# Kernel tuning notes

Measured on AMD Instinct MI355X. Metric: run time of the kernel, lower is better.

## Reference

```python
import jax, jax.numpy as jnp
import numpy as np

H, CM, CS = 8, 16, 32  # num_heads, hidden_mv_channels, hidden_s_channels
_INNER_IDX = np.array([0, 2, 3, 4, 8, 9, 10, 14])  # PGA multivector components without e0


def _make_basis():
    # 9 Pin(3,0,1)-equivariant linear maps on 16-dim multivectors:
    # 5 grade projections + 4 left-multiplications by e0 (grade k -> grade k+1 e0-blades).
    # Component order: [1, e0, e1, e2, e3, e01, e02, e03, e12, e13, e23, e012, e013, e023, e123, e0123]
    b = np.zeros((9, 16, 16), dtype=np.float32)
    grades = [[0], [1, 2, 3, 4], [5, 6, 7, 8, 9, 10], [11, 12, 13, 14], [15]]
    for k, idxs in enumerate(grades):
        for i in idxs:
            b[k, i, i] = 1.0
    e0maps = {5: [(0, 1)], 6: [(2, 5), (3, 6), (4, 7)], 7: [(8, 11), (9, 12), (10, 13)], 8: [(14, 15)]}
    for k, pairs in e0maps.items():
        for i, o in pairs:
            b[k, o, i] = 1.0
    return jnp.asarray(b)


BASIS = _make_basis()  # (9, 16_out_comp, 16_in_comp)


def equi_linear(mv, s, w_mv, w_s2mv, b_mv, w_mv2s, w_s2s, b_s):
    # mv: (..., c_in, 16); s: (..., s_in)
    out_mv = jnp.einsum('yai,ocy,...ci->...oa', BASIS, w_mv, mv)
    out_mv = out_mv.at[..., 0].add(jnp.einsum('...i,oi->...o', s, w_s2mv) + b_mv)
    out_s = (jnp.einsum('...c,sc->...s', mv[..., 0], w_mv2s)
             + jnp.einsum('...i,si->...s', s, w_s2s) + b_s)
    return out_mv, out_s


def reference(multivectors_kv, multivectors_q, scalars_kv, scalars_q,
              q_w_mv, q_w_s2mv, q_b_mv, q_w_mv2s, q_w_s2s, q_b_s,
              k_w_mv, k_w_s2mv, k_b_mv, k_w_mv2s, k_w_s2s, k_b_s,
              v_w_mv, v_w_s2mv, v_b_mv, v_w_mv2s, v_w_s2s, v_b_s,
              o_w_mv, o_w_s2mv, o_b_mv, o_w_mv2s, o_w_s2s, o_b_s):
    B, Q = multivectors_q.shape[0], multivectors_q.shape[1]
    q_mv, q_s = equi_linear(multivectors_q, scalars_q, q_w_mv, q_w_s2mv, q_b_mv, q_w_mv2s, q_w_s2s, q_b_s)
    k_mv, k_s = equi_linear(multivectors_kv, scalars_kv, k_w_mv, k_w_s2mv, k_b_mv, k_w_mv2s, k_w_s2s, k_b_s)
    v_mv, v_s = equi_linear(multivectors_kv, scalars_kv, v_w_mv, v_w_s2mv, v_b_mv, v_w_mv2s, v_w_s2s, v_b_s)
    # split heads; einops pattern '(hidden_channels num_heads)' => channel-major, head-minor
    q_mv = q_mv.reshape(B, Q, CM, H, 16).transpose(0, 3, 1, 2, 4)  # (B,H,Q,CM,16)
    q_s = q_s.reshape(B, Q, CS, H).transpose(0, 3, 1, 2)            # (B,H,Q,CS)
    # multi-query: single k/v head broadcast over H
    scale = 1.0 / jnp.sqrt(jnp.asarray(8 * CM + CS, dtype=q_mv.dtype))
    scores = (jnp.einsum('bhqcx,bkcx->bhqk', q_mv[..., _INNER_IDX], k_mv[..., _INNER_IDX])
              + jnp.einsum('bhqs,bks->bhqk', q_s, k_s)) * scale
    attn = jax.nn.softmax(scores, axis=-1)
    h_mv = jnp.einsum('bhqk,bkcx->bhqcx', attn, v_mv)
    h_s = jnp.einsum('bhqk,bkc->bhqc', attn, v_s)
    # merge heads; pattern '(n_heads hidden_channels)' => head-major
    h_mv = h_mv.transpose(0, 2, 1, 3, 4).reshape(B, Q, H * CM, 16)
    h_s = h_s.transpose(0, 2, 1, 3).reshape(B, Q, H * CS)
    out_mv, out_s = equi_linear(h_mv, h_s, o_w_mv, o_w_s2mv, o_b_mv, o_w_mv2s, o_w_s2s, o_b_s)
    return out_mv, out_s


def setup_inputs():
    key = jax.random.key(0)
    ks = jax.random.split(key, 32)
    B, NQ, NKV, IN_MV, IN_S = 4, 2048, 2048, 16, 32
    w = 0.05  # weight scale to keep attention logits sane

    def rn(k, shape, s=1.0):
        return jax.random.normal(k, shape, dtype=jnp.float32) * s

    return {
        'multivectors_kv': rn(ks[0], (B, NKV, IN_MV, 16)),
        'multivectors_q': rn(ks[1], (B, NQ, IN_MV, 16)),
        'scalars_kv': rn(ks[2], (B, NKV, IN_S)),
        'scalars_q': rn(ks[3], (B, NQ, IN_S)),
        'q_w_mv': rn(ks[4], (CM * H, IN_MV, 9), w),
        'q_w_s2mv': rn(ks[5], (CM * H, IN_S), w),
        'q_b_mv': jnp.zeros((CM * H,), jnp.float32),
        'q_w_mv2s': rn(ks[6], (CS * H, IN_MV), w),
        'q_w_s2s': rn(ks[7], (CS * H, IN_S), w),
        'q_b_s': jnp.zeros((CS * H,), jnp.float32),
        'k_w_mv': rn(ks[8], (CM, IN_MV, 9), w),
        'k_w_s2mv': rn(ks[9], (CM, IN_S), w),
        'k_b_mv': jnp.zeros((CM,), jnp.float32),
        'k_w_mv2s': rn(ks[10], (CS, IN_MV), w),
        'k_w_s2s': rn(ks[11], (CS, IN_S), w),
        'k_b_s': jnp.zeros((CS,), jnp.float32),
        'v_w_mv': rn(ks[12], (CM, IN_MV, 9), w),
        'v_w_s2mv': rn(ks[13], (CM, IN_S), w),
        'v_b_mv': jnp.zeros((CM,), jnp.float32),
        'v_w_mv2s': rn(ks[14], (CS, IN_MV), w),
        'v_w_s2s': rn(ks[15], (CS, IN_S), w),
        'v_b_s': jnp.zeros((CS,), jnp.float32),
        'o_w_mv': rn(ks[16], (16, CM * H, 9), w),
        'o_w_s2mv': rn(ks[17], (16, CS * H), w),
        'o_b_mv': jnp.zeros((16,), jnp.float32),
        'o_w_mv2s': rn(ks[18], (32, CM * H), w),
        'o_w_s2s': rn(ks[19], (32, CS * H), w),
        'o_b_s': jnp.zeros((32,), jnp.float32),
    }
```

## Files before the change

### kernel.cpp

```cpp
#include <hip/hip_runtime.h>
#include <hip/hip_bf16.h>
#include <math.h>

#define NB   4
#define NQL  2048
#define NKVL 2048
#define HN   8
#define DQK  160
#define DV   288
#define QT   256
#define KTL  64
#define KLP  168

#define SCALE 0.07905694150420949f

typedef __attribute__((ext_vector_type(8)))  short short8;
typedef __attribute__((ext_vector_type(4)))  float f32x4;
typedef __attribute__((ext_vector_type(16))) float f32x16;

__constant__ int c_grade[16] = {0,1,1,1,1,2,2,2,2,2,2,3,3,3,3,4};
__constant__ int c_inner[8]  = {0,2,3,4,8,9,10,14};
__constant__ int c_esrc[16]  = {-1,0,-1,-1,-1,2,3,4,-1,-1,-1,8,9,10,-1,14};
__constant__ int c_ey[16]    = {0,5,0,0,0,6,6,6,0,0,0,7,7,7,0,8};

__device__ __forceinline__ ushort f2bf(float v) {
  __hip_bfloat16 h = __float2bfloat16(v);
  union { __hip_bfloat16 b; ushort u; } cv; cv.b = h; return cv.u;
}

__device__ __forceinline__ void gload16(const void* g, void* l) {
  __builtin_amdgcn_global_load_lds(
      (const __attribute__((address_space(1))) unsigned int*)g,
      (__attribute__((address_space(3))) unsigned int*)l, 16, 0, 0);
}

#define KWMV   0
#define KS2MV  2304
#define KMV2S  2816
#define KS2S   3328
#define KBMV   4352
#define KBS    4368
#define VWMV   4400
#define VS2MV  6704
#define VMV2S  7216
#define VS2S   7728
#define VBMV   8752
#define VBS    8768
#define WLSZ   8800
#define XSTR   289
#define OSTR   456

__device__ __forceinline__ void kv_accum(const float* wL, const float* xL,
                                         int f, float acc[32]) {
  if (f < 160) {
    if (f < 128) {
      int c = f >> 3, a = c_inner[f & 7], y = c_grade[a];
      float bias = (a == 0) ? wL[KBMV + c] : 0.f;
#pragma unroll
      for (int p = 0; p < 32; p++) acc[p] = bias;
      for (int ci = 0; ci < 16; ci++) {
        float w = wL[KWMV + (c*16 + ci)*9 + y];
#pragma unroll
        for (int p = 0; p < 32; p++) acc[p] += w * xL[p*XSTR + ci*16 + a];
      }
      if (a == 0) {
        for (int i2 = 0; i2 < 32; i2++) {
          float w = wL[KS2MV + c*32 + i2];
#pragma unroll
          for (int p = 0; p < 32; p++) acc[p] += w * xL[p*XSTR + 256 + i2];
        }
      }
    } else {
      int si = f - 128;
      float bias = wL[KBS + si];
#pragma unroll
      for (int p = 0; p < 32; p++) acc[p] = bias;
      for (int ci = 0; ci < 16; ci++) {
        float w = wL[KMV2S + si*16 + ci];
#pragma unroll
        for (int p = 0; p < 32; p++) acc[p] += w * xL[p*XSTR + ci*16];
      }
      for (int i2 = 0; i2 < 32; i2++) {
        float w = wL[KS2S + si*32 + i2];
#pragma unroll
        for (int p = 0; p < 32; p++) acc[p] += w * xL[p*XSTR + 256 + i2];
      }
    }
  } else {
    int g = f - 160;
    if (g < 256) {
      int c = g >> 4, a = g & 15, y = c_grade[a];
      float bias = (a == 0) ? wL[VBMV + c] : 0.f;
#pragma unroll
      for (int p = 0; p < 32; p++) acc[p] = bias;
      for (int ci = 0; ci < 16; ci++) {
        float w = wL[VWMV + (c*16 + ci)*9 + y];
#pragma unroll
        for (int p = 0; p < 32; p++) acc[p] += w * xL[p*XSTR + ci*16 + a];
      }
      int sa = c_esrc[a];
      if (sa >= 0) {
        int ey = c_ey[a];
        for (int ci = 0; ci < 16; ci++) {
          float w = wL[VWMV + (c*16 + ci)*9 + ey];
#pragma unroll
          for (int p = 0; p < 32; p++) acc[p] += w * xL[p*XSTR + ci*16 + sa];
        }
      }
      if (a == 0) {
        for (int i2 = 0; i2 < 32; i2++) {
          float w = wL[VS2MV + c*32 + i2];
#pragma unroll
          for (int p = 0; p < 32; p++) acc[p] += w * xL[p*XSTR + 256 + i2];
        }
      }
    } else {
      int si = g - 256;
      float bias = wL[VBS + si];
#pragma unroll
      for (int p = 0; p < 32; p++) acc[p] = bias;
      for (int ci = 0; ci < 16; ci++) {
        float w = wL[VMV2S + si*16 + ci];
#pragma unroll
        for (int p = 0; p < 32; p++) acc[p] += w * xL[p*XSTR + ci*16];
      }
      for (int i2 = 0; i2 < 32; i2++) {
        float w = wL[VS2S + si*32 + i2];
#pragma unroll
        for (int p = 0; p < 32; p++) acc[p] += w * xL[p*XSTR + 256 + i2];
      }
    }
  }
}

__global__ __launch_bounds__(256) void proj_kv_kernel(
    const float* __restrict__ mv_kv, const float* __restrict__ s_kv,
    const float* __restrict__ kw_mv, const float* __restrict__ kw_s2mv, const float* __restrict__ kb_mv,
    const float* __restrict__ kw_mv2s, const float* __restrict__ kw_s2s, const float* __restrict__ kb_s,
    const float* __restrict__ vw_mv, const float* __restrict__ vw_s2mv, const float* __restrict__ vb_mv,
    const float* __restrict__ vw_mv2s, const float* __restrict__ vw_s2s, const float* __restrict__ vb_s,
    ushort* __restrict__ Kf, ushort* __restrict__ VfT)
{
  __shared__ float wL[WLSZ];
  __shared__ float xL[32*XSTR];
  int t = threadIdx.x;
  for (int i = t; i < 2304; i += 256) wL[KWMV + i] = kw_mv[i];
  for (int i = t; i < 512;  i += 256) wL[KS2MV + i] = kw_s2mv[i];
  for (int i = t; i < 512;  i += 256) wL[KMV2S + i] = kw_mv2s[i];
  for (int i = t; i < 1024; i += 256) wL[KS2S + i] = kw_s2s[i];
  if (t < 16) wL[KBMV + t] = kb_mv[t];
  if (t < 32) wL[KBS + t] = kb_s[t];
  for (int i = t; i < 2304; i += 256) wL[VWMV + i] = vw_mv[i];
  for (int i = t; i < 512;  i += 256) wL[VS2MV + i] = vw_s2mv[i];
  for (int i = t; i < 512;  i += 256) wL[VMV2S + i] = vw_mv2s[i];
  for (int i = t; i < 1024; i += 256) wL[VS2S + i] = vw_s2s[i];
  if (t < 16) wL[VBMV + t] = vb_mv[t];
  if (t < 32) wL[VBS + t] = vb_s[t];

  int p0 = blockIdx.x * 32;
  for (int i = t; i < 32*256; i += 256) {
    int p = i >> 8, c = i & 255;
    xL[p*XSTR + c] = mv_kv[(size_t)(p0 + p)*256 + c];
  }
  for (int i = t; i < 32*32; i += 256) {
    int p = i >> 5, c = i & 31;
    xL[p*XSTR + 256 + c] = s_kv[(size_t)(p0 + p)*32 + c];
  }
  __syncthreads();

  float acc0[32], acc1[32];
  kv_accum(wL, xL, t, acc0);
  if (t < 192) kv_accum(wL, xL, 256 + t, acc1);
  __syncthreads();

  ushort* oL = (ushort*)xL;
#pragma unroll
  for (int p = 0; p < 32; p++) oL[p*OSTR + t] = f2bf(acc0[p]);
  if (t < 192) {
#pragma unroll
    for (int p = 0; p < 32; p++) oL[p*OSTR + 256 + t] = f2bf(acc1[p]);
  }
  __syncthreads();

  int b = p0 >> 11, kv0 = p0 & 2047;
  for (int it = 0; it < 10; it++) {
    int j = t + it*256;
    int p = j / 80, fp = j - p*80;
    uint u = (uint)oL[p*OSTR + 2*fp] | ((uint)oL[p*OSTR + 2*fp + 1] << 16);
    *(uint*)(Kf + (size_t)(p0 + p)*DQK + 2*fp) = u;
  }
  for (int it = 0; it < 18; it++) {
    int j = t + it*256;
    int g = j >> 4, pp = j & 15;
    uint u = (uint)oL[(2*pp)*OSTR + 160 + g] | ((uint)oL[(2*pp+1)*OSTR + 160 + g] << 16);
    int kv = kv0 + 2*pp;
    int pos = (kv & ~63) + ((((kv >> 3) & 7) ^ (g & 7)) << 3) + (kv & 7);
    *(uint*)(VfT + ((size_t)b*DV + g)*NKVL + pos) = u;
  }
}

#define QWT_MV 0
#define QWT_S  20480
#define QBT    61440
#define QWT_SZ 62720
__global__ __launch_bounds__(256) void prep_qw_kernel(
    const float* __restrict__ qw_mv, const float* __restrict__ qw_s2mv, const float* __restrict__ qb_mv,
    const float* __restrict__ qw_mv2s, const float* __restrict__ qw_s2s, const float* __restrict__ qb_s,
    float* __restrict__ qwT)
{
  int i = blockIdx.x*256 + threadIdx.x;
  if (i >= QWT_SZ) return;
  if (i < QWT_S) {
    int ci = i / 1280, r = i - ci*1280, h = r / 160, f0 = r - h*160;
    float v;
    if (f0 < 128) {
      int c = f0 >> 3, a = c_inner[f0 & 7], y = c_grade[a];
      v = qw_mv[((c*HN + h)*16 + ci)*9 + y];
    } else {
      v = qw_mv2s[((f0 - 128)*HN + h)*16 + ci];
    }
    qwT[i] = v;
  } else if (i < QBT) {
    int j = i - QWT_S;
    int i2 = j / 1280, r = j - i2*1280, h = r / 160, f0 = r - h*160;
    float v;
    if (f0 < 128) {
      int c = f0 >> 3, a = c_inner[f0 & 7];
      v = (a == 0) ? qw_s2mv[(c*HN + h)*32 + i2] : 0.f;
    } else {
      v = qw_s2s[((f0 - 128)*HN + h)*32 + i2];
    }
    qwT[i] = v;
  } else {
    int r = i - QBT, h = r / 160, f0 = r - h*160;
    float v;
    if (f0 < 128) {
      int c = f0 >> 3, a = c_inner[f0 & 7];
      v = (a == 0) ? qb_mv[c*HN + h] : 0.f;
    } else {
      v = qb_s[(f0 - 128)*HN + h];
    }
    qwT[i] = v;
  }
}

__global__ __launch_bounds__(320) void proj_q_kernel(
    const float* __restrict__ mv_q, const float* __restrict__ s_q,
    const float* __restrict__ qwT,
    ushort* __restrict__ Qf)
{
  __shared__ float xL[16*XSTR];
  int t = threadIdx.x;
  int p0 = blockIdx.x * 16;
  for (int i = t; i < 16*256; i += 320) {
    int p = i >> 8, c = i & 255;
    xL[p*XSTR + c] = mv_q[(size_t)(p0 + p)*256 + c];
  }
  for (int i = t; i < 16*32; i += 320) {
    int p = i >> 5, c = i & 31;
    xL[p*XSTR + 256 + c] = s_q[(size_t)(p0 + p)*32 + c];
  }
  __syncthreads();

  int f0 = t % 160;
  int h0 = t / 160;
  int a = (f0 < 128) ? c_inner[f0 & 7] : 0;

  float acc[4][16];
#pragma unroll
  for (int k = 0; k < 4; k++) {
    float bv = qwT[QBT + (h0 + 2*k)*160 + f0];
#pragma unroll
    for (int p = 0; p < 16; p++) acc[k][p] = bv;
  }
  for (int ci = 0; ci < 16; ci++) {
    float w0 = qwT[QWT_MV + (ci*HN + h0    )*160 + f0];
    float w1 = qwT[QWT_MV + (ci*HN + h0 + 2)*160 + f0];
    float w2 = qwT[QWT_MV + (ci*HN + h0 + 4)*160 + f0];
    float w3 = qwT[QWT_MV + (ci*HN + h0 + 6)*160 + f0];
#pragma unroll
    for (int p = 0; p < 16; p++) {
      float xv = xL[p*XSTR + ci*16 + a];
      acc[0][p] += w0*xv; acc[1][p] += w1*xv;
      acc[2][p] += w2*xv; acc[3][p] += w3*xv;
    }
  }
  for (int i2 = 0; i2 < 32; i2++) {
    float w0 = qwT[QWT_S + (i2*HN + h0    )*160 + f0];
    float w1 = qwT[QWT_S + (i2*HN + h0 + 2)*160 + f0];
    float w2 = qwT[QWT_S + (i2*HN + h0 + 4)*160 + f0];
    float w3 = qwT[QWT_S + (i2*HN + h0 + 6)*160 + f0];
#pragma unroll
    for (int p = 0; p < 16; p++) {
      float xv = xL[p*XSTR + 256 + i2];
      acc[0][p] += w0*xv; acc[1][p] += w1*xv;
      acc[2][p] += w2*xv; acc[3][p] += w3*xv;
    }
  }

  int b = p0 >> 11, q0 = p0 & 2047;
#pragma unroll
  for (int k = 0; k < 4; k++) {
    int h = h0 + 2*k;
    ushort* qdst = Qf + ((size_t)(b*HN + h)*NQL + q0)*DQK + f0;
#pragma unroll
    for (int p = 0; p < 16; p++)
      qdst[p*DQK] = f2bf(acc[k][p] * SCALE);
  }
}

__global__ __launch_bounds__(512, 2) void attn_kernel(
    const ushort* __restrict__ Kf,
    const ushort* __restrict__ VfT,
    const ushort* __restrict__ Qf,
    float* __restrict__ Hf)
{
  __shared__ ushort kL[2][KTL*KLP];
  __shared__ ushort vtL[2][DV*KTL];

  const int NT = NQL/QT;
  int bid = blockIdx.x;
  int swz = (bid & 7) * 32 + (bid >> 3);
  int bh = swz / NT;
  int qt = swz - bh*NT;
  int b = bh >> 3, h = bh & 7;
  int t = threadIdx.x, w = t >> 6, l = t & 63;
  int ql = l & 31, hb = l >> 5;

  const ushort* kb = Kf  + (size_t)b*NKVL*DQK;
  const ushort* vb = VfT + (size_t)b*DV*NKVL;

  const ushort* qrow = Qf + ((size_t)bh*NQL + (size_t)qt*QT + w*32 + ql)*DQK + hb*8;
  short8 qf[10];
#pragma unroll
  for (int ks = 0; ks < 10; ks++)
    qf[ks] = *(const short8*)(qrow + ks*16);

  f32x16 oA[9];
#pragma unroll
  for (int i = 0; i < 9; i++) oA[i] = (f32x16)(0.f);
  float m = -INFINITY, lsum = 0.f;

#define STAGE(KT, BUF) do {                                            \
    const ushort* kg_ = kb + (size_t)(KT)*KTL*DQK;                     \
    char* kd_ = (char*)&kL[BUF][0];                                    \
    for (int c_ = w; c_ < 21; c_ += 8) {                               \
      int off_ = c_*1024 + l*16;                                       \
      int row_ = off_ / 336;                                           \
      int bc_  = off_ - row_*336;                                      \
      const ushort* ga_ = kg_ + row_*DQK + ((bc_ < 320) ? (bc_ >> 1) : 0); \
      gload16(ga_, kd_ + c_*1024);                                     \
    }                                                                  \
    const ushort* vg_ = vb + (size_t)(KT)*KTL;                         \
    char* vd_ = (char*)&vtL[BUF][0];                                   \
    for (int c_ = w; c_ < 36; c_ += 8) {                               \
      int off_ = c_*1024 + l*16;                                       \
      int d_  = off_ >> 7;                                             \
      int bc_ = off_ & 127;                                            \
      const ushort* ga_ = vg_ + (size_t)d_*NKVL + (bc_ >> 1);          \
      gload16(ga_, vd_ + c_*1024);                                     \
    }                                                                  \
  } while (0)

  STAGE(0, 0);
  __syncthreads();

  for (int kt = 0; kt < NKVL/KTL; kt++) {
    int cur = kt & 1;
    if (kt + 1 < NKVL/KTL) STAGE(kt + 1, cur ^ 1);

    const ushort* kbuf  = &kL[cur][0];
    const ushort* vtbuf = &vtL[cur][0];

    f32x16 sA[2];
    __builtin_amdgcn_s_setprio(1);
#pragma unroll
    for (int kvb = 0; kvb < 2; kvb++) {
      sA[kvb] = (f32x16)(0.f);
      const ushort* krow = kbuf + (ql + 32*kvb)*KLP + hb*8;
#pragma unroll
      for (int ks = 0; ks < 10; ks++) {
        short8 kf = *(const short8*)(krow + ks*16);
        sA[kvb] = __builtin_amdgcn_mfma_f32_32x32x16_bf16(kf, qf[ks], sA[kvb], 0, 0, 0);
      }
    }
    __builtin_amdgcn_s_setprio(0);

    float tm = sA[0][0];
#pragma unroll
    for (int kvb = 0; kvb < 2; kvb++)
#pragma unroll
      for (int r = 0; r < 16; r++) tm = fmaxf(tm, sA[kvb][r]);
    tm = fmaxf(tm, __shfl_xor(tm, 32));
    if (!__all(tm - m <= 8.0f)) {
      float nm = fmaxf(m, tm);
      float ef = __expf(m - nm);
      lsum *= ef;
#pragma unroll
      for (int i = 0; i < 9; i++)
#pragma unroll
        for (int r = 0; r < 16; r++) oA[i][r] *= ef;
      m = nm;
    }
    float rs = 0.f;
#pragma unroll
    for (int kvb = 0; kvb < 2; kvb++)
#pragma unroll
      for (int r = 0; r < 16; r++) {
        float p = __expf(sA[kvb][r] - m);
        sA[kvb][r] = p;
        rs += p;
      }
    rs += __shfl_xor(rs, 32);
    lsum += rs;

    unsigned int pk[2][8];
#pragma unroll
    for (int kvb = 0; kvb < 2; kvb++)
#pragma unroll
      for (int k = 0; k < 8; k++) {
        unsigned int r_;
        asm("v_cvt_pk_bf16_f32 %0, %1, %2" : "=v"(r_) : "v"(sA[kvb][2*k]), "v"(sA[kvb][2*k+1]));
        pk[kvb][k] = r_;
      }

#pragma unroll
    for (int s = 0; s < 4; s++) {
      const int n0 = 2*s, n1 = 2*s + 1;
      unsigned int u[4];
#pragma unroll
      for (int p = 0; p < 4; p++) {
        unsigned int Xa = pk[n0 >> 2][(p & 1) + 2*(n0 & 3)];
        unsigned int Xb = pk[n1 >> 2][(p & 1) + 2*(n1 & 3)];
        int src = ql + 32*(p >> 1);
        unsigned int ua = __shfl((int)Xa, src);
        unsigned int ub = __shfl((int)Xb, src);
        u[p] = hb ? ub : ua;
      }
      union { unsigned int uu[4]; short8 s8; } pf;
      pf.uu[0] = u[0]; pf.uu[1] = u[1]; pf.uu[2] = u[2]; pf.uu[3] = u[3];
      __builtin_amdgcn_s_setprio(1);
#pragma unroll
      for (int db = 0; db < 9; db++) {
        int d = ql + 32*db;
        int col = (((2*s + hb) ^ (d & 7)) << 3);
        short8 vf = *(const short8*)(vtbuf + d*KTL + col);
        oA[db] = __builtin_amdgcn_mfma_f32_32x32x16_bf16(vf, pf.s8, oA[db], 0, 0, 0);
      }
      __builtin_amdgcn_s_setprio(0);
    }
    __syncthreads();
  }
#undef STAGE

  float inv = 1.0f / lsum;
  int q = qt*QT + w*32 + ql;
  float* orow = Hf + (((size_t)b*NQL + q)*HN + h)*DV;
#pragma unroll
  for (int db = 0; db < 9; db++)
#pragma unroll
    for (int j = 0; j < 4; j++) {
      int d0 = 32*db + 8*j + 4*hb;
      float4 st = make_float4(oA[db][4*j]*inv, oA[db][4*j+1]*inv,
                              oA[db][4*j+2]*inv, oA[db][4*j+3]*inv);
      *(float4*)(orow + d0) = st;
    }
}

#define OWT_SZ 34816
__global__ __launch_bounds__(256) void prep_ow_kernel(
    const float* __restrict__ ow_mv, const float* __restrict__ ow_s2mv,
    const float* __restrict__ ow_mv2s, const float* __restrict__ ow_s2s,
    float* __restrict__ owT)
{
  int i = blockIdx.x*256 + threadIdx.x;
  if (i < 18432) {
    int y = i / 2048, r = i & 2047, ch = r >> 4, o = r & 15;
    owT[i] = ow_mv[(size_t)(o*128 + ch)*9 + y];
  } else if (i < 22528) {
    int r = i - 18432, jj = r >> 4, o = r & 15;
    owT[i] = ow_s2mv[o*256 + jj];
  } else if (i < 26624) {
    int r = i - 22528, ch = r >> 5, si = r & 31;
    owT[i] = ow_mv2s[si*128 + ch];
  } else if (i < OWT_SZ) {
    int r = i - 26624, jj = r >> 5, si = r & 31;
    owT[i] = ow_s2s[si*256 + jj];
  }
}

#define HSTR 2308
__global__ __launch_bounds__(256) void proj_o_kernel(
    const float* __restrict__ Hf,
    const float* __restrict__ owT,
    const float* __restrict__ ob_mv, const float* __restrict__ ob_s,
    float* __restrict__ outp)
{
  __shared__ float hL[8*HSTR];
  int t = threadIdx.x;
  int p0 = blockIdx.x * 8;
  for (int i = t; i < 8*2304/4; i += 256) {
    int idx = i*4; int p = idx / 2304; int c = idx - p*2304;
    *(float4*)(hL + p*HSTR + c) = *(const float4*)(Hf + (size_t)(p0 + p)*2304 + c);
  }
  __syncthreads();

  const float* mvT   = owT;
  const float* s2mvT = owT + 18432;
  const float* mv2sT = owT + 22528;
  const float* s2sT  = owT + 26624;

  int o = t & 15, pp = (t >> 4) & 7, half = t >> 7;
  const float* x = hL + pp*HSTR;
  float acc[8];
#pragma unroll
  for (int a = 0; a < 8; a++) acc[a] = 0.f;
  if (half == 0) acc[0] = ob_mv[o];

  if (half == 0) {
    for (int ch = 0; ch < 128; ch++) {
      const float* xc = x + (ch >> 4)*288 + (ch & 15)*16;
      float w0 = mvT[0*2048 + ch*16 + o], w1 = mvT[1*2048 + ch*16 + o];
      float w2 = mvT[2*2048 + ch*16 + o];
      float w5 = mvT[5*2048 + ch*16 + o], w6 = mvT[6*2048 + ch*16 + o];
      float x0 = xc[0], x1 = xc[1], x2 = xc[2], x3 = xc[3];
      float x4 = xc[4], x5 = xc[5], x6 = xc[6], x7 = xc[7];
      acc[0] += w0*x0;
      acc[1] += w1*x1 + w5*x0;
      acc[2] += w1*x2;
      acc[3] += w1*x3;
      acc[4] += w1*x4;
      acc[5] += w2*x5 + w6*x2;
      acc[6] += w2*x6 + w6*x3;
      acc[7] += w2*x7 + w6*x4;
    }
    for (int jj = 0; jj < 256; jj++)
      acc[0] += s2mvT[jj*16 + o] * x[(jj >> 5)*288 + 256 + (jj & 31)];
  } else {
    for (int ch = 0; ch < 128; ch++) {
      const float* xc = x + (ch >> 4)*288 + (ch & 15)*16 + 8;
      float w2 = mvT[2*2048 + ch*16 + o], w3 = mvT[3*2048 + ch*16 + o];
      float w4 = mvT[4*2048 + ch*16 + o];
      float w7 = mvT[7*2048 + ch*16 + o], w8 = mvT[8*2048 + ch*16 + o];
      float x8 = xc[0], x9 = xc[1], x10 = xc[2], x11 = xc[3];
      float x12 = xc[4], x13 = xc[5], x14 = xc[6], x15 = xc[7];
      acc[0] += w2*x8;
      acc[1] += w2*x9;
      acc[2] += w2*x10;
      acc[3] += w3*x11 + w7*x8;
      acc[4] += w3*x12 + w7*x9;
      acc[5] += w3*x13 + w7*x10;
      acc[6] += w3*x14;
      acc[7] += w4*x15 + w8*x14;
    }
  }

  float* od = outp + (size_t)(p0 + pp)*256 + o*16 + half*8;
  *(float4*)(od)     = make_float4(acc[0], acc[1], acc[2], acc[3]);
  *(float4*)(od + 4) = make_float4(acc[4], acc[5], acc[6], acc[7]);

  int si = t & 31, ps = t >> 5;
  const float* xs = hL + ps*HSTR;
  float vs = ob_s[si];
  for (int ch = 0; ch < 128; ch++)
    vs += mv2sT[ch*32 + si] * xs[(ch >> 4)*288 + (ch & 15)*16];
  for (int jj = 0; jj < 256; jj++)
    vs += s2sT[jj*32 + si] * xs[(jj >> 5)*288 + 256 + (jj & 31)];
  float* out_s = outp + (size_t)NB*NQL*256;
  out_s[(size_t)(p0 + ps)*32 + si] = vs;
}

extern "C" void kernel_launch(void* const* d_in, const int* in_sizes, int n_in,
                              void* d_out, int out_size, void* d_ws, size_t ws_size,
                              hipStream_t stream)
{
  const float* mv_kv = (const float*)d_in[0];
  const float* mv_q  = (const float*)d_in[1];
  const float* s_kv  = (const float*)d_in[2];
  const float* s_q   = (const float*)d_in[3];

  ushort* Kf  = (ushort*)d_ws;
  ushort* VfT = Kf  + (size_t)NB*NKVL*DQK;
  ushort* Qf  = VfT + (size_t)NB*DV*NKVL;
  float*  Hf  = (float*)(Qf + (size_t)NB*HN*NQL*DQK);
  float*  owT = Hf + (size_t)NB*NQL*HN*DV;
  float*  qwT = owT + OWT_SZ;

  prep_ow_kernel<<<(OWT_SZ + 255)/256, 256, 0, stream>>>(
      (const float*)d_in[22], (const float*)d_in[23],
      (const float*)d_in[25], (const float*)d_in[26], owT);
  prep_qw_kernel<<<(QWT_SZ + 255)/256, 256, 0, stream>>>(
      (const float*)d_in[4], (const float*)d_in[5], (const float*)d_in[6],
      (const float*)d_in[7], (const float*)d_in[8], (const float*)d_in[9],
      qwT);
  proj_kv_kernel<<<NB*NKVL/32, 256, 0, stream>>>(mv_kv, s_kv,
      (const float*)d_in[10], (const float*)d_in[11], (const float*)d_in[12],
      (const float*)d_in[13], (const float*)d_in[14], (const float*)d_in[15],
      (const float*)d_in[16], (const float*)d_in[17], (const float*)d_in[18],
      (const float*)d_in[19], (const float*)d_in[20], (const float*)d_in[21],
      Kf, VfT);
  proj_q_kernel<<<NB*NQL/16, 320, 0, stream>>>(mv_q, s_q, qwT, Qf);
  attn_kernel<<<NB*HN*(NQL/QT), 512, 0, stream>>>(Kf, VfT, Qf, Hf);
  proj_o_kernel<<<NB*NQL/8, 256, 0, stream>>>(Hf, owT,
      (const float*)d_in[24], (const float*)d_in[27],
      (float*)d_out);
}
```

Before: 370.3 us.

## Shrink per-block positions in projections, split output reduction, merge weight prep kernels

Cuts positions per block in the KV projection (32 to 8) and Q projection (16 to 8), giving more blocks, fewer registers per thread and less shared memory. The output projection now handles 4 positions per block and splits the channel reduction into two segments whose partial sums are combined through shared memory. The two weight-prep kernels are merged into one launch. The aim is better occupancy and less launch overhead, at the cost of reloading weights into shared memory in more blocks and an extra sync and reduction step.

```diff
diff --git a/kernel.cpp b/kernel.cpp
--- a/kernel.cpp
+++ b/kernel.cpp
@@ -49,41 +49,42 @@
 #define WLSZ   8800
 #define XSTR   289
 #define OSTR   456
+#define KVPOS  8
 
 __device__ __forceinline__ void kv_accum(const float* wL, const float* xL,
-                                         int f, float acc[32]) {
+                                         int f, float acc[KVPOS]) {
   if (f < 160) {
     if (f < 128) {
       int c = f >> 3, a = c_inner[f & 7], y = c_grade[a];
       float bias = (a == 0) ? wL[KBMV + c] : 0.f;
 #pragma unroll
-      for (int p = 0; p < 32; p++) acc[p] = bias;
+      for (int p = 0; p < KVPOS; p++) acc[p] = bias;
       for (int ci = 0; ci < 16; ci++) {
         float w = wL[KWMV + (c*16 + ci)*9 + y];
 #pragma unroll
-        for (int p = 0; p < 32; p++) acc[p] += w * xL[p*XSTR + ci*16 + a];
+        for (int p = 0; p < KVPOS; p++) acc[p] += w * xL[p*XSTR + ci*16 + a];
       }
       if (a == 0) {
         for (int i2 = 0; i2 < 32; i2++) {
           float w = wL[KS2MV + c*32 + i2];
 #pragma unroll
-          for (int p = 0; p < 32; p++) acc[p] += w * xL[p*XSTR + 256 + i2];
+          for (int p = 0; p < KVPOS; p++) acc[p] += w * xL[p*XSTR + 256 + i2];
         }
       }
     } else {
       int si = f - 128;
       float bias = wL[KBS + si];
 #pragma unroll
-      for (int p = 0; p < 32; p++) acc[p] = bias;
+      for (int p = 0; p < KVPOS; p++) acc[p] = bias;
       for (int ci = 0; ci < 16; ci++) {
         float w = wL[KMV2S + si*16 + ci];
 #pragma unroll
-        for (int p = 0; p < 32; p++) acc[p] += w * xL[p*XSTR + ci*16];
+        for (int p = 0; p < KVPOS; p++) acc[p] += w * xL[p*XSTR + ci*16];
       }
       for (int i2 = 0; i2 < 32; i2++) {
         float w = wL[KS2S + si*32 + i2];
 #pragma unroll
-        for (int p = 0; p < 32; p++) acc[p] += w * xL[p*XSTR + 256 + i2];
+        for (int p = 0; p < KVPOS; p++) acc[p] += w * xL[p*XSTR + 256 + i2];
       }
     }
   } else {
@@ -92,11 +93,11 @@
       int c = g >> 4, a = g & 15, y = c_grade[a];
       float bias = (a == 0) ? wL[VBMV + c] : 0.f;
 #pragma unroll
-      for (int p = 0; p < 32; p++) acc[p] = bias;
+      for (int p = 0; p < KVPOS; p++) acc[p] = bias;
       for (int ci = 0; ci < 16; ci++) {
         float w = wL[VWMV + (c*16 + ci)*9 + y];
 #pragma unroll
-        for (int p = 0; p < 32; p++) acc[p] += w * xL[p*XSTR + ci*16 + a];
+        for (int p = 0; p < KVPOS; p++) acc[p] += w * xL[p*XSTR + ci*16 + a];
       }
       int sa = c_esrc[a];
       if (sa >= 0) {
@@ -104,30 +105,30 @@
         for (int ci = 0; ci < 16; ci++) {
           float w = wL[VWMV + (c*16 + ci)*9 + ey];
 #pragma unroll
-          for (int p = 0; p < 32; p++) acc[p] += w * xL[p*XSTR + ci*16 + sa];
+          for (int p = 0; p < KVPOS; p++) acc[p] += w * xL[p*XSTR + ci*16 + sa];
         }
       }
       if (a == 0) {
         for (int i2 = 0; i2 < 32; i2++) {
           float w = wL[VS2MV + c*32 + i2];
 #pragma unroll
-          for (int p = 0; p < 32; p++) acc[p] += w * xL[p*XSTR + 256 + i2];
+          for (int p = 0; p < KVPOS; p++) acc[p] += w * xL[p*XSTR + 256 + i2];
         }
       }
     } else {
       int si = g - 256;
       float bias = wL[VBS + si];
 #pragma unroll
-      for (int p = 0; p < 32; p++) acc[p] = bias;
+      for (int p = 0; p < KVPOS; p++) acc[p] = bias;
       for (int ci = 0; ci < 16; ci++) {
         float w = wL[VMV2S + si*16 + ci];
 #pragma unroll
-        for (int p = 0; p < 32; p++) acc[p] += w * xL[p*XSTR + ci*16];
+        for (int p = 0; p < KVPOS; p++) acc[p] += w * xL[p*XSTR + ci*16];
       }
       for (int i2 = 0; i2 < 32; i2++) {
         float w = wL[VS2S + si*32 + i2];
 #pragma unroll
-        for (int p = 0; p < 32; p++) acc[p] += w * xL[p*XSTR + 256 + i2];
+        for (int p = 0; p < KVPOS; p++) acc[p] += w * xL[p*XSTR + 256 + i2];
       }
     }
   }
@@ -142,7 +143,7 @@
     ushort* __restrict__ Kf, ushort* __restrict__ VfT)
 {
   __shared__ float wL[WLSZ];
-  __shared__ float xL[32*XSTR];
+  __shared__ float xL[KVPOS*XSTR];
   int t = threadIdx.x;
   for (int i = t; i < 2304; i += 256) wL[KWMV + i] = kw_mv[i];
   for (int i = t; i < 512;  i += 256) wL[KS2MV + i] = kw_s2mv[i];
@@ -157,61 +158,86 @@
   if (t < 16) wL[VBMV + t] = vb_mv[t];
   if (t < 32) wL[VBS + t] = vb_s[t];
 
-  int p0 = blockIdx.x * 32;
-  for (int i = t; i < 32*256; i += 256) {
+  int p0 = blockIdx.x * KVPOS;
+  for (int i = t; i < KVPOS*256; i += 256) {
     int p = i >> 8, c = i & 255;
     xL[p*XSTR + c] = mv_kv[(size_t)(p0 + p)*256 + c];
   }
-  for (int i = t; i < 32*32; i += 256) {
-    int p = i >> 5, c = i & 31;
+  if (t < KVPOS*32) {
+    int p = t >> 5, c = t & 31;
     xL[p*XSTR + 256 + c] = s_kv[(size_t)(p0 + p)*32 + c];
   }
   __syncthreads();
 
-  float acc0[32], acc1[32];
+  float acc0[KVPOS], acc1[KVPOS];
   kv_accum(wL, xL, t, acc0);
   if (t < 192) kv_accum(wL, xL, 256 + t, acc1);
   __syncthreads();
 
   ushort* oL = (ushort*)xL;
 #pragma unroll
-  for (int p = 0; p < 32; p++) oL[p*OSTR + t] = f2bf(acc0[p]);
+  for (int p = 0; p < KVPOS; p++) oL[p*OSTR + t] = f2bf(acc0[p]);
   if (t < 192) {
 #pragma unroll
-    for (int p = 0; p < 32; p++) oL[p*OSTR + 256 + t] = f2bf(acc1[p]);
+    for (int p = 0; p < KVPOS; p++) oL[p*OSTR + 256 + t] = f2bf(acc1[p]);
   }
   __syncthreads();
 
   int b = p0 >> 11, kv0 = p0 & 2047;
-  for (int it = 0; it < 10; it++) {
+  for (int it = 0; it < 3; it++) {
     int j = t + it*256;
-    int p = j / 80, fp = j - p*80;
-    uint u = (uint)oL[p*OSTR + 2*fp] | ((uint)oL[p*OSTR + 2*fp + 1] << 16);
-    *(uint*)(Kf + (size_t)(p0 + p)*DQK + 2*fp) = u;
-  }
-  for (int it = 0; it < 18; it++) {
+    if (j < KVPOS*80) {
+      int p = j / 80, fp = j - p*80;
+      uint u = (uint)oL[p*OSTR + 2*fp] | ((uint)oL[p*OSTR + 2*fp + 1] << 16);
+      *(uint*)(Kf + (size_t)(p0 + p)*DQK + 2*fp) = u;
+    }
+  }
+  for (int it = 0; it < 5; it++) {
     int j = t + it*256;
-    int g = j >> 4, pp = j & 15;
-    uint u = (uint)oL[(2*pp)*OSTR + 160 + g] | ((uint)oL[(2*pp+1)*OSTR + 160 + g] << 16);
-    int kv = kv0 + 2*pp;
-    int pos = (kv & ~63) + ((((kv >> 3) & 7) ^ (g & 7)) << 3) + (kv & 7);
-    *(uint*)(VfT + ((size_t)b*DV + g)*NKVL + pos) = u;
-  }
-}
-
+    if (j < DV*(KVPOS/2)) {
+      int g = j >> 2, pp = j & 3;
+      uint u = (uint)oL[(2*pp)*OSTR + 160 + g] | ((uint)oL[(2*pp+1)*OSTR + 160 + g] << 16);
+      int kv = kv0 + 2*pp;
+      int pos = (kv & ~63) + ((((kv >> 3) & 7) ^ (g & 7)) << 3) + (kv & 7);
+      *(uint*)(VfT + ((size_t)b*DV + g)*NKVL + pos) = u;
+    }
+  }
+}
+
+#define OWT_SZ 34816
 #define QWT_MV 0
 #define QWT_S  20480
 #define QBT    61440
 #define QWT_SZ 62720
-__global__ __launch_bounds__(256) void prep_qw_kernel(
+__global__ __launch_bounds__(256) void prep_w_kernel(
+    const float* __restrict__ ow_mv, const float* __restrict__ ow_s2mv,
+    const float* __restrict__ ow_mv2s, const float* __restrict__ ow_s2s,
+    float* __restrict__ owT,
     const float* __restrict__ qw_mv, const float* __restrict__ qw_s2mv, const float* __restrict__ qb_mv,
     const float* __restrict__ qw_mv2s, const float* __restrict__ qw_s2s, const float* __restrict__ qb_s,
     float* __restrict__ qwT)
 {
   int i = blockIdx.x*256 + threadIdx.x;
-  if (i >= QWT_SZ) return;
-  if (i < QWT_S) {
-    int ci = i / 1280, r = i - ci*1280, h = r / 160, f0 = r - h*160;
+  if (i < OWT_SZ) {
+    if (i < 18432) {
+      int y = i / 2048, r = i & 2047, ch = r >> 4, o = r & 15;
+      owT[i] = ow_mv[(size_t)(o*128 + ch)*9 + y];
+    } else if (i < 22528) {
+      int r = i - 18432, jj = r >> 4, o = r & 15;
+      owT[i] = ow_s2mv[o*256 + jj];
+    } else if (i < 26624) {
+      int r = i - 22528, ch = r >> 5, si = r & 31;
+      owT[i] = ow_mv2s[si*128 + ch];
+    } else {
+      int r = i - 26624, jj = r >> 5, si = r & 31;
+      owT[i] = ow_s2s[si*256 + jj];
+    }
+    return;
+  }
+  int j = i - OWT_SZ;
+  if (j >= QWT_SZ) return;
+  if (j < QWT_S) {
+    int ci = j / 1280, r = j - ci*1280, h = r / 160, f0 = r - h*160;
     float v;
     if (f0 < 128) {
       int c = f0 >> 3, a = c_inner[f0 & 7], y = c_grade[a];
@@ -219,10 +245,10 @@
     } else {
       v = qw_mv2s[((f0 - 128)*HN + h)*16 + ci];
     }
-    qwT[i] = v;
-  } else if (i < QBT) {
-    int j = i - QWT_S;
-    int i2 = j / 1280, r = j - i2*1280, h = r / 160, f0 = r - h*160;
+    qwT[j] = v;
+  } else if (j < QBT) {
+    int k = j - QWT_S;
+    int i2 = k / 1280, r = k - i2*1280, h = r / 160, f0 = r - h*160;
     float v;
     if (f0 < 128) {
       int c = f0 >> 3, a = c_inner[f0 & 7];
@@ -230,9 +256,9 @@
     } else {
       v = qw_s2s[((f0 - 128)*HN + h)*32 + i2];
     }
-    qwT[i] = v;
+    qwT[j] = v;
   } else {
-    int r = i - QBT, h = r / 160, f0 = r - h*160;
+    int r = j - QBT, h = r / 160, f0 = r - h*160;
     float v;
     if (f0 < 128) {
       int c = f0 >> 3, a = c_inner[f0 & 7];
@@ -240,24 +266,25 @@
     } else {
       v = qb_s[(f0 - 128)*HN + h];
     }
-    qwT[i] = v;
-  }
-}
-
+    qwT[j] = v;
+  }
+}
+
+#define QPOS 8
 __global__ __launch_bounds__(320) void proj_q_kernel(
     const float* __restrict__ mv_q, const float* __restrict__ s_q,
     const float* __restrict__ qwT,
     ushort* __restrict__ Qf)
 {
-  __shared__ float xL[16*XSTR];
+  __shared__ float xL[QPOS*XSTR];
   int t = threadIdx.x;
-  int p0 = blockIdx.x * 16;
-  for (int i = t; i < 16*256; i += 320) {
+  int p0 = blockIdx.x * QPOS;
+  for (int i = t; i < QPOS*256; i += 320) {
     int p = i >> 8, c = i & 255;
     xL[p*XSTR + c] = mv_q[(size_t)(p0 + p)*256 + c];
   }
-  for (int i = t; i < 16*32; i += 320) {
-    int p = i >> 5, c = i & 31;
+  if (t < QPOS*32) {
+    int p = t >> 5, c = t & 31;
     xL[p*XSTR + 256 + c] = s_q[(size_t)(p0 + p)*32 + c];
   }
   __syncthreads();
@@ -266,12 +293,12 @@
   int h0 = t / 160;
   int a = (f0 < 128) ? c_inner[f0 & 7] : 0;
 
-  float acc[4][16];
+  float acc[4][QPOS];
 #pragma unroll
   for (int k = 0; k < 4; k++) {
     float bv = qwT[QBT + (h0 + 2*k)*160 + f0];
 #pragma unroll
-    for (int p = 0; p < 16; p++) acc[k][p] = bv;
+    for (int p = 0; p < QPOS; p++) acc[k][p] = bv;
   }
   for (int ci = 0; ci < 16; ci++) {
     float w0 = qwT[QWT_MV + (ci*HN + h0    )*160 + f0];
@@ -279,7 +306,7 @@
     float w2 = qwT[QWT_MV + (ci*HN + h0 + 4)*160 + f0];
     float w3 = qwT[QWT_MV + (ci*HN + h0 + 6)*160 + f0];
 #pragma unroll
-    for (int p = 0; p < 16; p++) {
+    for (int p = 0; p < QPOS; p++) {
       float xv = xL[p*XSTR + ci*16 + a];
       acc[0][p] += w0*xv; acc[1][p] += w1*xv;
       acc[2][p] += w2*xv; acc[3][p] += w3*xv;
@@ -291,7 +318,7 @@
     float w2 = qwT[QWT_S + (i2*HN + h0 + 4)*160 + f0];
     float w3 = qwT[QWT_S + (i2*HN + h0 + 6)*160 + f0];
 #pragma unroll
-    for (int p = 0; p < 16; p++) {
+    for (int p = 0; p < QPOS; p++) {
       float xv = xL[p*XSTR + 256 + i2];
       acc[0][p] += w0*xv; acc[1][p] += w1*xv;
       acc[2][p] += w2*xv; acc[3][p] += w3*xv;
@@ -304,7 +331,7 @@
     int h = h0 + 2*k;
     ushort* qdst = Qf + ((size_t)(b*HN + h)*NQL + q0)*DQK + f0;
 #pragma unroll
-    for (int p = 0; p < 16; p++)
+    for (int p = 0; p < QPOS; p++)
       qdst[p*DQK] = f2bf(acc[k][p] * SCALE);
   }
 }
@@ -467,39 +494,20 @@
     }
 }
 
-#define OWT_SZ 34816
-__global__ __launch_bounds__(256) void prep_ow_kernel(
-    const float* __restrict__ ow_mv, const float* __restrict__ ow_s2mv,
-    const float* __restrict__ ow_mv2s, const float* __restrict__ ow_s2s,
-    float* __restrict__ owT)
-{
-  int i = blockIdx.x*256 + threadIdx.x;
-  if (i < 18432) {
-    int y = i / 2048, r = i & 2047, ch = r >> 4, o = r & 15;
-    owT[i] = ow_mv[(size_t)(o*128 + ch)*9 + y];
-  } else if (i < 22528) {
-    int r = i - 18432, jj = r >> 4, o = r & 15;
-    owT[i] = ow_s2mv[o*256 + jj];
-  } else if (i < 26624) {
-    int r = i - 22528, ch = r >> 5, si = r & 31;
-    owT[i] = ow_mv2s[si*128 + ch];
-  } else if (i < OWT_SZ) {
-    int r = i - 26624, jj = r >> 5, si = r & 31;
-    owT[i] = ow_s2s[si*256 + jj];
-  }
-}
-
 #define HSTR 2308
+#define OPOS 4
 __global__ __launch_bounds__(256) void proj_o_kernel(
     const float* __restrict__ Hf,
     const float* __restrict__ owT,
     const float* __restrict__ ob_mv, const float* __restrict__ ob_s,
     float* __restrict__ outp)
 {
-  __shared__ float hL[8*HSTR];
+  __shared__ float hL[OPOS*HSTR];
+  __shared__ float pL[128*8];
+  __shared__ float sP[128];
   int t = threadIdx.x;
-  int p0 = blockIdx.x * 8;
-  for (int i = t; i < 8*2304/4; i += 256) {
+  int p0 = blockIdx.x * OPOS;
+  for (int i = t; i < OPOS*2304/4; i += 256) {
     int idx = i*4; int p = idx / 2304; int c = idx - p*2304;
     *(float4*)(hL + p*HSTR + c) = *(const float4*)(Hf + (size_t)(p0 + p)*2304 + c);
   }
@@ -510,15 +518,16 @@
   const float* mv2sT = owT + 22528;
   const float* s2sT  = owT + 26624;
 
-  int o = t & 15, pp = (t >> 4) & 7, half = t >> 7;
+  int o = t & 15, pp = (t >> 4) & 3, half = (t >> 6) & 1, seg = t >> 7;
   const float* x = hL + pp*HSTR;
   float acc[8];
 #pragma unroll
   for (int a = 0; a < 8; a++) acc[a] = 0.f;
-  if (half == 0) acc[0] = ob_mv[o];
+  if (half == 0 && seg == 0) acc[0] = ob_mv[o];
+  int ch0 = seg*64;
 
   if (half == 0) {
-    for (int ch = 0; ch < 128; ch++) {
+    for (int ch = ch0; ch < ch0 + 64; ch++) {
       const float* xc = x + (ch >> 4)*288 + (ch & 15)*16;
       float w0 = mvT[0*2048 + ch*16 + o], w1 = mvT[1*2048 + ch*16 + o];
       float w2 = mvT[2*2048 + ch*16 + o];
@@ -534,10 +543,10 @@
       acc[6] += w2*x6 + w6*x3;
       acc[7] += w2*x7 + w6*x4;
     }
-    for (int jj = 0; jj < 256; jj++)
+    for (int jj = seg*128; jj < seg*128 + 128; jj++)
       acc[0] += s2mvT[jj*16 + o] * x[(jj >> 5)*288 + 256 + (jj & 31)];
   } else {
-    for (int ch = 0; ch < 128; ch++) {
+    for (int ch = ch0; ch < ch0 + 64; ch++) {
       const float* xc = x + (ch >> 4)*288 + (ch & 15)*16 + 8;
       float w2 = mvT[2*2048 + ch*16 + o], w3 = mvT[3*2048 + ch*16 + o];
       float w4 = mvT[4*2048 + ch*16 + o];
@@ -555,19 +564,32 @@
     }
   }
 
-  float* od = outp + (size_t)(p0 + pp)*256 + o*16 + half*8;
-  *(float4*)(od)     = make_float4(acc[0], acc[1], acc[2], acc[3]);
-  *(float4*)(od + 4) = make_float4(acc[4], acc[5], acc[6], acc[7]);
-
-  int si = t & 31, ps = t >> 5;
+  int si = t & 31, ps = (t >> 5) & 3;
   const float* xs = hL + ps*HSTR;
-  float vs = ob_s[si];
-  for (int ch = 0; ch < 128; ch++)
+  float vs = (seg == 0) ? ob_s[si] : 0.f;
+  for (int ch = seg*64; ch < seg*64 + 64; ch++)
     vs += mv2sT[ch*32 + si] * xs[(ch >> 4)*288 + (ch & 15)*16];
-  for (int jj = 0; jj < 256; jj++)
+  for (int jj = seg*128; jj < seg*128 + 128; jj++)
     vs += s2sT[jj*32 + si] * xs[(jj >> 5)*288 + 256 + (jj & 31)];
-  float* out_s = outp + (size_t)NB*NQL*256;
-  out_s[(size_t)(p0 + ps)*32 + si] = vs;
+
+  if (seg == 1) {
+    float* pd = pL + ((half*4 + pp)*16 + o)*8;
+#pragma unroll
+    for (int a = 0; a < 8; a++) pd[a] = acc[a];
+    sP[ps*32 + si] = vs;
+  }
+  __syncthreads();
+  if (seg == 0) {
+    const float* pd = pL + ((half*4 + pp)*16 + o)*8;
+#pragma unroll
+    for (int a = 0; a < 8; a++) acc[a] += pd[a];
+    float* od = outp + (size_t)(p0 + pp)*256 + o*16 + half*8;
+    *(float4*)(od)     = make_float4(acc[0], acc[1], acc[2], acc[3]);
+    *(float4*)(od + 4) = make_float4(acc[4], acc[5], acc[6], acc[7]);
+    vs += sP[ps*32 + si];
+    float* out_s = outp + (size_t)NB*NQL*256;
+    out_s[(size_t)(p0 + ps)*32 + si] = vs;
+  }
 }
 
 extern "C" void kernel_launch(void* const* d_in, const int* in_sizes, int n_in,
@@ -586,22 +608,21 @@
   float*  owT = Hf + (size_t)NB*NQL*HN*DV;
   float*  qwT = owT + OWT_SZ;
 
-  prep_ow_kernel<<<(OWT_SZ + 255)/256, 256, 0, stream>>>(
+  prep_w_kernel<<<(OWT_SZ + QWT_SZ + 255)/256, 256, 0, stream>>>(
       (const float*)d_in[22], (const float*)d_in[23],
-      (const float*)d_in[25], (const float*)d_in[26], owT);
-  prep_qw_kernel<<<(QWT_SZ + 255)/256, 256, 0, stream>>>(
+      (const float*)d_in[25], (const float*)d_in[26], owT,
       (const float*)d_in[4], (const float*)d_in[5], (const float*)d_in[6],
       (const float*)d_in[7], (const float*)d_in[8], (const float*)d_in[9],
       qwT);
-  proj_kv_kernel<<<NB*NKVL/32, 256, 0, stream>>>(mv_kv, s_kv,
+  proj_kv_kernel<<<NB*NKVL/KVPOS, 256, 0, stream>>>(mv_kv, s_kv,
       (const float*)d_in[10], (const float*)d_in[11], (const float*)d_in[12],
       (const float*)d_in[13], (const float*)d_in[14], (const float*)d_in[15],
       (const float*)d_in[16], (const float*)d_in[17], (const float*)d_in[18],
       (const float*)d_in[19], (const float*)d_in[20], (const float*)d_in[21],
       Kf, VfT);
-  proj_q_kernel<<<NB*NQL/16, 320, 0, stream>>>(mv_q, s_q, qwT, Qf);
+  proj_q_kernel<<<NB*NQL/QPOS, 320, 0, stream>>>(mv_q, s_q, qwT, Qf);
   attn_kernel<<<NB*HN*(NQL/QT), 512, 0, stream>>>(Kf, VfT, Qf, Hf);
-  proj_o_kernel<<<NB*NQL/8, 256, 0, stream>>>(Hf, owT,
+  proj_o_kernel<<<NB*NQL/OPOS, 256, 0, stream>>>(Hf, owT,
       (const float*)d_in[24], (const float*)d_in[27],
       (float*)d_out);
 }
```

After: 385.7 us. 1.04x slower.
